# Performance work log

Measured on AMD Instinct MI355X. Metric: run time of the kernel, lower is better.

Reference implementation:

```python
import jax, jax.numpy as jnp
import numpy as np

N_HEADS = 16
EPSILON = 0.01
SCORE_SCALE = 1.0
C_CONST = 2.0 + EPSILON


def setup_inputs() -> dict:
    key = jax.random.key(0)
    k1, k2, k3 = jax.random.split(key, 3)
    B, T, D = 2, 2048, 1024
    x = jax.random.normal(k1, (B, T, D), dtype=jnp.float32)
    # torch nn.Linear convention: weight [out_features, in_features], y = x @ W.T
    Wqkv = jax.random.normal(k2, (3 * D, D), dtype=jnp.float32) * (1.0 / np.sqrt(D))
    Wout = jax.random.normal(k3, (D, D), dtype=jnp.float32) * (1.0 / np.sqrt(D))
    return {"x": x, "Wqkv": Wqkv, "Wout": Wout}


def reference(x, Wqkv, Wout):
    B, T, D = x.shape
    H = N_HEADS
    hd = D // H
    qkv = x @ Wqkv.T  # [B, T, 3D]
    q, k, v = jnp.split(qkv, 3, axis=-1)
    # [B, H, T, hd]
    q = q.reshape(B, T, H, hd).transpose(0, 2, 1, 3).astype(jnp.float32)
    k = k.reshape(B, T, H, hd).transpose(0, 2, 1, 3).astype(jnp.float32)
    v = v.reshape(B, T, H, hd).transpose(0, 2, 1, 3).astype(jnp.float32)
    # L2 normalize along head dim (F.normalize uses eps=1e-12 via clamp of norm)
    qn = q / jnp.maximum(jnp.linalg.norm(q, axis=-1, keepdims=True), 1e-12)
    kn = k / jnp.maximum(jnp.linalg.norm(k, axis=-1, keepdims=True), 1e-12)
    # full T x T kernel matrix per (batch, head)
    x_dot = jnp.einsum("bhtd,bhsd->bhts", qn, kn)
    denom = jnp.maximum(C_CONST - 2.0 * x_dot, 1e-6)
    K = (x_dot * x_dot) / denom * SCORE_SCALE
    causal = jnp.tril(jnp.ones((T, T), dtype=bool))  # keep lower triangle incl. diag
    K = jnp.where(causal[None, None, :, :], K, 0.0)
    numerator = jnp.einsum("bhts,bhsd->bhtd", K, v)
    denominator = jnp.sum(K, axis=-1, keepdims=True)
    out = numerator / (denominator + 1e-6)
    out = out.transpose(0, 2, 1, 3).reshape(B, T, D)
    return out @ Wout.T
```

## Files before the change

### kernel.cpp

```cpp
#include <hip/hip_runtime.h>
#include <hip/hip_bf16.h>

#define T_SEQ 2048
#define D_MODEL 1024
#define BT 4096
#define QKV_N 3072

typedef __attribute__((ext_vector_type(8))) short bf16x8;
typedef __attribute__((ext_vector_type(4))) short bf16x4;
typedef __attribute__((ext_vector_type(4))) float f32x4;

typedef unsigned int __attribute__((address_space(1))) as1_uint;
typedef unsigned int __attribute__((address_space(3))) as3_uint;

__device__ __forceinline__ unsigned short f2bf(float f) {
    unsigned u = __builtin_bit_cast(unsigned, f);
    u += 0x7fffu + ((u >> 16) & 1u);
    return (unsigned short)(u >> 16);
}
__device__ __forceinline__ float bf2f(unsigned short h) {
    unsigned u = ((unsigned)h) << 16;
    return __builtin_bit_cast(float, u);
}
__device__ __forceinline__ void gload_lds16(const void* g, void* l) {
    __builtin_amdgcn_global_load_lds((const as1_uint*)g, (as3_uint*)l, 16, 0, 0);
}
__device__ __forceinline__ unsigned cvtpk_bf16(float lo, float hi) {
    unsigned r;
    asm("v_cvt_pk_bf16_f32 %0, %1, %2" : "=v"(r) : "v"(lo), "v"(hi));
    return r;
}

__global__ __launch_bounds__(256) void cvt_bf16_3(const float* __restrict__ s0, unsigned short* __restrict__ d0, int n0,
                                                  const float* __restrict__ s1, unsigned short* __restrict__ d1, int n1,
                                                  const float* __restrict__ s2, unsigned short* __restrict__ d2, int n2) {
    int i = blockIdx.x * 256 + threadIdx.x;
    const float* s; unsigned short* d;
    if (i < n0) { s = s0; d = d0; }
    else if (i < n0 + n1) { i -= n0; s = s1; d = d1; }
    else if (i < n0 + n1 + n2) { i -= n0 + n1; s = s2; d = d2; }
    else return;
    const float4* sp = (const float4*)s + (size_t)i * 2;
    const float4 a = sp[0], b = sp[1];
    uint4 o;
    o.x = (unsigned)f2bf(a.x) | ((unsigned)f2bf(a.y) << 16);
    o.y = (unsigned)f2bf(a.z) | ((unsigned)f2bf(a.w) << 16);
    o.z = (unsigned)f2bf(b.x) | ((unsigned)f2bf(b.y) << 16);
    o.w = (unsigned)f2bf(b.z) | ((unsigned)f2bf(b.w) << 16);
    ((uint4*)d)[i] = o;
}

template<int MODE>
__global__ __launch_bounds__(256) void gemm_bt_mfma(const unsigned short* __restrict__ A,
                                                    const unsigned short* __restrict__ B,
                                                    void* __restrict__ Cout,
                                                    unsigned short* __restrict__ qbp,
                                                    unsigned short* __restrict__ kbp,
                                                    int M, int N, int K) {
    __shared__ unsigned short As[128 * 64];
    __shared__ unsigned short Bs[128 * 64];
    const int tid = threadIdx.x;
    const int w = tid >> 6;
    const int l = tid & 63;
    const int l15 = l & 15, l4 = l >> 4;

    const int nblocks = (M / 128) * (N / 128);
    const int cpx = nblocks >> 3;
    const int id2 = (blockIdx.x & 7) * cpx + (blockIdx.x >> 3);
    const int bm = (id2 & 31) * 128;
    const int bn = (id2 >> 5) * 128;

    const int wm = (w >> 1) * 64, wn = (w & 1) * 64;

    const f32x4 z = {0.f, 0.f, 0.f, 0.f};
    f32x4 acc[4][4];
#pragma unroll
    for (int m = 0; m < 4; ++m)
#pragma unroll
        for (int n = 0; n < 4; ++n) acc[m][n] = z;

    const int lrow = l >> 3;
    const int lslot = (l & 7) ^ (lrow & 7);

    for (int k0 = 0; k0 < K; k0 += 64) {
#pragma unroll
        for (int i = 0; i < 4; ++i) {
            const int row = w * 32 + i * 8 + lrow;
            gload_lds16(A + (size_t)(bm + row) * K + k0 + lslot * 8, As + (w * 4 + i) * 512);
            gload_lds16(B + (size_t)(bn + row) * K + k0 + lslot * 8, Bs + (w * 4 + i) * 512);
        }
        __syncthreads();
        bf16x8 af[4][2], bfr[4][2];
#pragma unroll
        for (int m = 0; m < 4; ++m) {
            const int row = wm + m * 16 + l15;
            af[m][0] = *(const bf16x8*)(As + row * 64 + ((l4 ^ (row & 7)) * 8));
            af[m][1] = *(const bf16x8*)(As + row * 64 + (((4 + l4) ^ (row & 7)) * 8));
        }
#pragma unroll
        for (int n = 0; n < 4; ++n) {
            const int row = wn + n * 16 + l15;
            bfr[n][0] = *(const bf16x8*)(Bs + row * 64 + ((l4 ^ (row & 7)) * 8));
            bfr[n][1] = *(const bf16x8*)(Bs + row * 64 + (((4 + l4) ^ (row & 7)) * 8));
        }
#pragma unroll
        for (int m = 0; m < 4; ++m)
#pragma unroll
            for (int n = 0; n < 4; ++n) {
                acc[m][n] = __builtin_amdgcn_mfma_f32_16x16x32_bf16(af[m][0], bfr[n][0], acc[m][n], 0, 0, 0);
                acc[m][n] = __builtin_amdgcn_mfma_f32_16x16x32_bf16(af[m][1], bfr[n][1], acc[m][n], 0, 0, 0);
            }
        __syncthreads();
    }

    if (MODE == 0) {
#pragma unroll
        for (int m = 0; m < 4; ++m)
#pragma unroll
            for (int n = 0; n < 4; ++n)
#pragma unroll
                for (int r = 0; r < 4; ++r) {
                    const int row = bm + wm + m * 16 + l4 * 4 + r;
                    const int col = bn + wn + n * 16 + l15;
                    ((float*)Cout)[(size_t)row * N + col] = acc[m][n][r];
                }
    } else {
        const int gcol0 = bn + wn;
        const int part = gcol0 >> 10;
        const int h = (gcol0 >> 6) & 15;
        if (part < 2) {
            unsigned short* dst = part ? kbp : qbp;
#pragma unroll
            for (int m = 0; m < 4; ++m)
#pragma unroll
                for (int r = 0; r < 4; ++r) {
                    float ss = 0.f;
#pragma unroll
                    for (int n = 0; n < 4; ++n) ss = fmaf(acc[m][n][r], acc[m][n][r], ss);
                    ss += __shfl_xor(ss, 1);
                    ss += __shfl_xor(ss, 2);
                    ss += __shfl_xor(ss, 4);
                    ss += __shfl_xor(ss, 8);
                    const float sc = 1.0f / fmaxf(sqrtf(ss), 1e-12f);
                    const int row = bm + wm + m * 16 + l4 * 4 + r;
                    const int bh2 = (row >> 11) * 16 + h;
                    unsigned short* pdst = dst + ((size_t)bh2 * T_SEQ + (row & 2047)) * 64 + l15;
#pragma unroll
                    for (int n = 0; n < 4; ++n) pdst[n * 16] = f2bf(acc[m][n][r] * sc);
                }
        } else {
            unsigned short* vrow = (unsigned short*)Cout;
            const int vcol0 = gcol0 - 2048;
#pragma unroll
            for (int m = 0; m < 4; ++m)
#pragma unroll
                for (int n = 0; n < 4; ++n)
#pragma unroll
                    for (int r = 0; r < 4; ++r) {
                        const int row = bm + wm + m * 16 + l4 * 4 + r;
                        vrow[(size_t)row * D_MODEL + vcol0 + n * 16 + l15] = f2bf(acc[m][n][r]);
                    }
        }
    }
}

__global__ __launch_bounds__(256) void v_cvt_T(const unsigned short* __restrict__ vrow,
                                               unsigned short* __restrict__ vbT) {
    __shared__ unsigned short tile[64][72];
    const int bh = blockIdx.y;
    const int b = bh >> 4, h = bh & 15;
    const int t0 = blockIdx.x * 64;
    const int r = threadIdx.x >> 2;
    const int c = (threadIdx.x & 3) * 16;
    const unsigned short* src = vrow + (size_t)(b * T_SEQ + t0 + r) * D_MODEL + h * 64 + c;
    uint4 v0 = *(const uint4*)(src);
    uint4 v1 = *(const uint4*)(src + 8);
    unsigned short tmp[16];
    *(uint4*)tmp = v0;
    *(uint4*)(tmp + 8) = v1;
#pragma unroll
    for (int j = 0; j < 16; ++j) tile[c + j][r] = tmp[j];
    __syncthreads();
    const int d = threadIdx.x >> 2;
    const int tc = (threadIdx.x & 3) * 16;
    const int t5 = tc >> 5, t4 = (tc >> 4) & 1;
    unsigned short* dstrow = vbT + ((size_t)bh * 64 + d) * T_SEQ + t0;
    const int dp = d & 7;
#pragma unroll
    for (int q = 0; q < 4; ++q) {
        unsigned short tmp2[4];
#pragma unroll
        for (int i = 0; i < 4; ++i) tmp2[i] = tile[d][tc + q * 4 + i];
        const int slot = (t5 * 4 + q) ^ dp;
        *(uint2*)(dstrow + slot * 8 + t4 * 4) = *(uint2*)tmp2;
    }
}

#define AT_TS 64

__global__ __launch_bounds__(256, 4) void attn_mfma(const unsigned short* __restrict__ qb,
                                                    const unsigned short* __restrict__ kb,
                                                    const unsigned short* __restrict__ vbT,
                                                    unsigned short* __restrict__ attnb) {
    __shared__ unsigned short Ks[2][64 * 64];
    __shared__ unsigned short Vs[2][64 * 64];

    const int tid = threadIdx.x;
    const int w = tid >> 6;
    const int l = tid & 63;
    const int l15 = l & 15, l4 = l >> 4;

    const int id = blockIdx.x;
    const int xcd = id & 7;
    const int within = id >> 3;
    const int hl = (((within >> 5) & 1) << 1) | (within & 1);
    const int vv = (((within >> 6) & 1) << 4) | (((within >> 4) & 1) << 3) |
                   (((within >> 3) & 1) << 2) | (((within >> 2) & 1) << 1) |
                   ((within >> 1) & 1);
    const int pfl = ((within >> 5) & 1) ^ (within & 1);
    const int bh = xcd * 4 + hl;
    const int t0i = pfl ? 31 - vv : vv;
    const int t0 = t0i * 64;

    const size_t hb = (size_t)bh * T_SEQ * 64;

    const int lrow = l >> 3;
    const int lslot = (l & 7) ^ (lrow & 7);
    const unsigned short* kgp[2];
    const unsigned short* vgp[2];
    unsigned short* kdst[2];
    unsigned short* vdst[2];
#pragma unroll
    for (int c = 0; c < 2; ++c) {
        const int row = w * 16 + c * 8 + lrow;
        kgp[c] = kb + hb + (size_t)row * 64 + lslot * 8;
        vgp[c] = vbT + hb + (size_t)row * T_SEQ + (l & 7) * 8;
        kdst[c] = &Ks[0][(w * 2 + c) * 512];
        vdst[c] = &Vs[0][(w * 2 + c) * 512];
    }

    const int p = l15 & 7;
    const unsigned short* kfp0 = &Ks[0][0] + l15 * 64 + ((l4 ^ p) * 8);
    const unsigned short* kfp1 = &Ks[0][0] + l15 * 64 + (((4 + l4) ^ p) * 8);
    const unsigned short* vfp0 = &Vs[0][0] + l15 * 64 + ((l4 ^ p) * 8);
    const unsigned short* vfp1 = &Vs[0][0] + l15 * 64 + (((4 + l4) ^ p) * 8);

    bf16x8 qf0, qf1;
    {
        const unsigned short* qp = qb + hb + (size_t)(t0 + w * 16 + l15) * 64 + l4 * 8;
        qf0 = *(const bf16x8*)(qp);
        qf1 = *(const bf16x8*)(qp + 32);
    }

    const f32x4 z = {0.f, 0.f, 0.f, 0.f};
    f32x4 acc[4];
#pragma unroll
    for (int i = 0; i < 4; ++i) acc[i] = z;
    float accd = 0.f;

    const int wrow0 = t0 + w * 16;
    const int tq = wrow0 + l15;

#pragma unroll
    for (int c = 0; c < 2; ++c) {
        gload_lds16(kgp[c], kdst[c]);
        gload_lds16(vgp[c], vdst[c]);
    }

    auto compute_tile = [&](int roff, int s0, bool mask) {
        const unsigned short* kc0 = kfp0 + roff;
        const unsigned short* kc1 = kfp1 + roff;
        f32x4 sC[4];
        __builtin_amdgcn_s_setprio(1);
#pragma unroll
        for (int sf = 0; sf < 4; ++sf) {
            bf16x8 kf0 = *(const bf16x8*)(kc0 + sf * 1024);
            bf16x8 kf1 = *(const bf16x8*)(kc1 + sf * 1024);
            f32x4 c = z;
            c = __builtin_amdgcn_mfma_f32_16x16x32_bf16(kf0, qf0, c, 0, 0, 0);
            c = __builtin_amdgcn_mfma_f32_16x16x32_bf16(kf1, qf1, c, 0, 0, 0);
            sC[sf] = c;
        }
        __builtin_amdgcn_s_setprio(0);
        float part_ = 0.f;
#pragma unroll
        for (int sf = 0; sf < 4; ++sf)
#pragma unroll
            for (int r = 0; r < 4; ++r) {
                const float xd = sC[sf][r];
                const float den = __builtin_fmaf(-2.0f, xd, 2.01f);
                float Kv = xd * xd * __builtin_amdgcn_rcpf(den);
                if (mask) {
                    const int s = s0 + sf * 16 + l4 * 4 + r;
                    if (s > tq) Kv = 0.f;
                }
                part_ += Kv;
                sC[sf][r] = Kv;
            }
        accd += part_;
        uint4 p0, p1;
        p0.x = cvtpk_bf16(sC[0][0], sC[0][1]);
        p0.y = cvtpk_bf16(sC[0][2], sC[0][3]);
        p0.z = cvtpk_bf16(sC[1][0], sC[1][1]);
        p0.w = cvtpk_bf16(sC[1][2], sC[1][3]);
        p1.x = cvtpk_bf16(sC[2][0], sC[2][1]);
        p1.y = cvtpk_bf16(sC[2][2], sC[2][3]);
        p1.z = cvtpk_bf16(sC[3][0], sC[3][1]);
        p1.w = cvtpk_bf16(sC[3][2], sC[3][3]);
        const bf16x8 a0 = __builtin_bit_cast(bf16x8, p0);
        const bf16x8 a1 = __builtin_bit_cast(bf16x8, p1);
        const unsigned short* vc0 = vfp0 + roff;
        const unsigned short* vc1 = vfp1 + roff;
        __builtin_amdgcn_s_setprio(1);
#pragma unroll
        for (int df = 0; df < 4; ++df) {
            const bf16x8 B0 = *(const bf16x8*)(vc0 + df * 1024);
            const bf16x8 B1 = *(const bf16x8*)(vc1 + df * 1024);
            acc[df] = __builtin_amdgcn_mfma_f32_16x16x32_bf16(a0, B0, acc[df], 0, 0, 0);
            acc[df] = __builtin_amdgcn_mfma_f32_16x16x32_bf16(a1, B1, acc[df], 0, 0, 0);
        }
        __builtin_amdgcn_s_setprio(0);
    };

    for (int st = 0; st < t0i; ++st) {
        const int dsto = ((st & 1) ^ 1) * 4096;
#pragma unroll
        for (int c = 0; c < 2; ++c) {
            kgp[c] += 4096;
            vgp[c] += 64;
            gload_lds16(kgp[c], kdst[c] + dsto);
            gload_lds16(vgp[c], vdst[c] + dsto);
        }
        asm volatile("s_waitcnt vmcnt(4)" ::: "memory");
        __builtin_amdgcn_sched_barrier(0);
        __builtin_amdgcn_s_barrier();
        compute_tile((st & 1) * 4096, st * AT_TS, false);
        __builtin_amdgcn_sched_barrier(0);
        __builtin_amdgcn_s_barrier();
    }
    {
        asm volatile("s_waitcnt vmcnt(0)" ::: "memory");
        __builtin_amdgcn_sched_barrier(0);
        __builtin_amdgcn_s_barrier();
        compute_tile((t0i & 1) * 4096, t0i * AT_TS, true);
    }

    accd += __shfl_xor(accd, 16);
    accd += __shfl_xor(accd, 32);

    const int b = bh >> 4, h = bh & 15;
#pragma unroll
    for (int r = 0; r < 4; ++r) {
        const float den = __shfl(accd, l4 * 4 + r) + 1e-6f;
#pragma unroll
        for (int df = 0; df < 4; ++df) {
            const int t = wrow0 + l4 * 4 + r;
            const float o = acc[df][r] / den;
            attnb[((size_t)b * T_SEQ + t) * D_MODEL + h * 64 + df * 16 + l15] = f2bf(o);
        }
    }
}

extern "C" void kernel_launch(void* const* d_in, const int* in_sizes, int n_in,
                              void* d_out, int out_size, void* d_ws, size_t ws_size,
                              hipStream_t stream) {
    const float* x    = (const float*)d_in[0];
    const float* Wqkv = (const float*)d_in[1];
    const float* Wout = (const float*)d_in[2];
    float* out = (float*)d_out;

    char* ws = (char*)d_ws;
    unsigned short* xb    = (unsigned short*)(ws);
    unsigned short* wqkvb = (unsigned short*)(ws + (size_t)8 * 1024 * 1024);
    unsigned short* vrow  = (unsigned short*)(ws + (size_t)16 * 1024 * 1024);
    unsigned short* vbT   = (unsigned short*)(ws + (size_t)24 * 1024 * 1024);
    unsigned short* woutb = (unsigned short*)(ws + (size_t)32 * 1024 * 1024);
    unsigned short* qbp   = (unsigned short*)(ws + (size_t)34 * 1024 * 1024);
    unsigned short* kbp   = (unsigned short*)(ws + (size_t)42 * 1024 * 1024);
    unsigned short* attnb = (unsigned short*)(ws + (size_t)50 * 1024 * 1024);

    cvt_bf16_3<<<4096, 256, 0, stream>>>(x, xb, BT * D_MODEL / 8,
                                         Wqkv, wqkvb, QKV_N * D_MODEL / 8,
                                         Wout, woutb, D_MODEL * D_MODEL / 8);

    gemm_bt_mfma<2><<<(QKV_N / 128) * (BT / 128), 256, 0, stream>>>(
        xb, wqkvb, vrow, qbp, kbp, BT, QKV_N, D_MODEL);

    v_cvt_T<<<dim3(T_SEQ / 64, 32), 256, 0, stream>>>(vrow, vbT);

    attn_mfma<<<1024, 256, 0, stream>>>(qbp, kbp, vbT, attnb);

    gemm_bt_mfma<0><<<(D_MODEL / 128) * (BT / 128), 256, 0, stream>>>(
        attnb, woutb, out, nullptr, nullptr, BT, D_MODEL, D_MODEL);
}
```

Measured before the change: 179.3 us.

## Split long causal attention rows into two KV chunks with a reduction kernel

The causal attention kernel now splits each query tile at positions 16 and above into two key/value chunks (split-K), so no block processes more than 16 KV tiles. A static task table orders the work longest-first to balance load across the 1536 blocks. The partial numerators (bf16) and denominators go to reused workspace buffers, and a new attn_reduce kernel combines and normalizes them. This adds an extra launch, extra memory traffic and bf16 rounding of the partial numerators.

```diff
diff --git a/kernel.cpp b/kernel.cpp
--- a/kernel.cpp
+++ b/kernel.cpp
@@ -198,10 +198,22 @@
 
 #define AT_TS 64
 
+static __device__ const unsigned char task_tab[48] = {
+    (15<<1)|0,(16<<1)|0,(17<<1)|0,(18<<1)|0,(19<<1)|0,(20<<1)|0,(21<<1)|0,(22<<1)|0,
+    (23<<1)|0,(24<<1)|0,(25<<1)|0,(26<<1)|0,(27<<1)|0,(28<<1)|0,(29<<1)|0,(30<<1)|0,
+    (31<<1)|0,(31<<1)|1,
+    (14<<1)|0,(30<<1)|1,(13<<1)|0,(29<<1)|1,(12<<1)|0,(28<<1)|1,(11<<1)|0,(27<<1)|1,
+    (10<<1)|0,(26<<1)|1,(9<<1)|0,(25<<1)|1,(8<<1)|0,(24<<1)|1,(7<<1)|0,(23<<1)|1,
+    (6<<1)|0,(22<<1)|1,(5<<1)|0,(21<<1)|1,(4<<1)|0,(20<<1)|1,(3<<1)|0,(19<<1)|1,
+    (2<<1)|0,(18<<1)|1,(1<<1)|0,(17<<1)|1,(0<<1)|0,(16<<1)|1,
+};
+
 __global__ __launch_bounds__(256, 4) void attn_mfma(const unsigned short* __restrict__ qb,
                                                     const unsigned short* __restrict__ kb,
                                                     const unsigned short* __restrict__ vbT,
-                                                    unsigned short* __restrict__ attnb) {
+                                                    unsigned short* __restrict__ attnb,
+                                                    unsigned short* __restrict__ pnum,
+                                                    float* __restrict__ pden) {
     __shared__ unsigned short Ks[2][64 * 64];
     __shared__ unsigned short Vs[2][64 * 64];
 
@@ -212,15 +224,17 @@
 
     const int id = blockIdx.x;
     const int xcd = id & 7;
-    const int within = id >> 3;
-    const int hl = (((within >> 5) & 1) << 1) | (within & 1);
-    const int vv = (((within >> 6) & 1) << 4) | (((within >> 4) & 1) << 3) |
-                   (((within >> 3) & 1) << 2) | (((within >> 2) & 1) << 1) |
-                   ((within >> 1) & 1);
-    const int pfl = ((within >> 5) & 1) ^ (within & 1);
+    const int wq = id >> 3;
+    const int hl = wq & 3;
+    const int task = wq >> 2;
     const int bh = xcd * 4 + hl;
-    const int t0i = pfl ? 31 - vv : vv;
-    const int t0 = t0i * 64;
+    const int tv = task_tab[task];
+    const int j = tv >> 1;
+    const int chunk = tv & 1;
+    const int nst = chunk ? (j - 15) : (j < 16 ? j + 1 : 16);
+    const bool mfin = chunk ? true : (j < 16);
+    const int s_base = chunk * 16;
+    const int t0 = j * 64;
 
     const size_t hb = (size_t)bh * T_SEQ * 64;
 
@@ -233,8 +247,8 @@
 #pragma unroll
     for (int c = 0; c < 2; ++c) {
         const int row = w * 16 + c * 8 + lrow;
-        kgp[c] = kb + hb + (size_t)row * 64 + lslot * 8;
-        vgp[c] = vbT + hb + (size_t)row * T_SEQ + (l & 7) * 8;
+        kgp[c] = kb + hb + (size_t)(s_base * 64 + row) * 64 + lslot * 8;
+        vgp[c] = vbT + hb + (size_t)row * T_SEQ + s_base * 64 + (l & 7) * 8;
         kdst[c] = &Ks[0][(w * 2 + c) * 512];
         vdst[c] = &Vs[0][(w * 2 + c) * 512];
     }
@@ -322,7 +336,7 @@
         __builtin_amdgcn_s_setprio(0);
     };
 
-    for (int st = 0; st < t0i; ++st) {
+    for (int st = 0; st < nst - 1; ++st) {
         const int dsto = ((st & 1) ^ 1) * 4096;
 #pragma unroll
         for (int c = 0; c < 2; ++c) {
@@ -334,7 +348,7 @@
         asm volatile("s_waitcnt vmcnt(4)" ::: "memory");
         __builtin_amdgcn_sched_barrier(0);
         __builtin_amdgcn_s_barrier();
-        compute_tile((st & 1) * 4096, st * AT_TS, false);
+        compute_tile((st & 1) * 4096, (s_base + st) * AT_TS, false);
         __builtin_amdgcn_sched_barrier(0);
         __builtin_amdgcn_s_barrier();
     }
@@ -342,23 +356,62 @@
         asm volatile("s_waitcnt vmcnt(0)" ::: "memory");
         __builtin_amdgcn_sched_barrier(0);
         __builtin_amdgcn_s_barrier();
-        compute_tile((t0i & 1) * 4096, t0i * AT_TS, true);
+        compute_tile(((nst - 1) & 1) * 4096, (s_base + nst - 1) * AT_TS, mfin);
     }
 
     accd += __shfl_xor(accd, 16);
     accd += __shfl_xor(accd, 32);
 
+    if (!chunk && j < 16) {
+        const int b = bh >> 4, h = bh & 15;
+#pragma unroll
+        for (int r = 0; r < 4; ++r) {
+            const float den = __shfl(accd, l4 * 4 + r) + 1e-6f;
+#pragma unroll
+            for (int df = 0; df < 4; ++df) {
+                const int t = wrow0 + l4 * 4 + r;
+                const float o = acc[df][r] / den;
+                attnb[((size_t)b * T_SEQ + t) * D_MODEL + h * 64 + df * 16 + l15] = f2bf(o);
+            }
+        }
+    } else {
+        const int pj = j - 16;
+        const int pidx = (bh * 16 + pj) * 2 + chunk;
+        unsigned short* np = pnum + (size_t)pidx * 4096;
+#pragma unroll
+        for (int r = 0; r < 4; ++r)
+#pragma unroll
+            for (int df = 0; df < 4; ++df)
+                np[(w * 16 + l4 * 4 + r) * 64 + df * 16 + l15] = f2bf(acc[df][r]);
+        if (l4 == 0) pden[pidx * 64 + w * 16 + l15] = accd;
+    }
+}
+
+__global__ __launch_bounds__(256) void attn_reduce(const unsigned short* __restrict__ pnum,
+                                                   const float* __restrict__ pden,
+                                                   unsigned short* __restrict__ attnb) {
+    const int bh = blockIdx.y;
+    const int jj = blockIdx.x;
+    const int row = threadIdx.x >> 2;
+    const int d0 = (threadIdx.x & 3) * 16;
+    const int pi = (bh * 16 + jj) * 2;
+    const float den = pden[pi * 64 + row] + pden[(pi + 1) * 64 + row] + 1e-6f;
+    const float inv = 1.0f / den;
+    const unsigned short* n0 = pnum + (size_t)pi * 4096 + row * 64 + d0;
+    const unsigned short* n1 = n0 + 4096;
     const int b = bh >> 4, h = bh & 15;
-#pragma unroll
-    for (int r = 0; r < 4; ++r) {
-        const float den = __shfl(accd, l4 * 4 + r) + 1e-6f;
-#pragma unroll
-        for (int df = 0; df < 4; ++df) {
-            const int t = wrow0 + l4 * 4 + r;
-            const float o = acc[df][r] / den;
-            attnb[((size_t)b * T_SEQ + t) * D_MODEL + h * 64 + df * 16 + l15] = f2bf(o);
-        }
-    }
+    unsigned short* dst = attnb + ((size_t)b * T_SEQ + (16 + jj) * 64 + row) * D_MODEL + h * 64 + d0;
+    uint4 a0 = *(const uint4*)n0, a1 = *(const uint4*)(n0 + 8);
+    uint4 c0 = *(const uint4*)n1, c1 = *(const uint4*)(n1 + 8);
+    unsigned short sa[8], sb[8], o[16];
+    *(uint4*)sa = a0; *(uint4*)sb = c0;
+#pragma unroll
+    for (int i = 0; i < 8; ++i) o[i] = f2bf((bf2f(sa[i]) + bf2f(sb[i])) * inv);
+    *(uint4*)sa = a1; *(uint4*)sb = c1;
+#pragma unroll
+    for (int i = 0; i < 8; ++i) o[8 + i] = f2bf((bf2f(sa[i]) + bf2f(sb[i])) * inv);
+    *(uint4*)dst = *(uint4*)o;
+    *(uint4*)(dst + 8) = *(uint4*)(o + 8);
 }
 
 extern "C" void kernel_launch(void* const* d_in, const int* in_sizes, int n_in,
@@ -378,6 +431,8 @@
     unsigned short* qbp   = (unsigned short*)(ws + (size_t)34 * 1024 * 1024);
     unsigned short* kbp   = (unsigned short*)(ws + (size_t)42 * 1024 * 1024);
     unsigned short* attnb = (unsigned short*)(ws + (size_t)50 * 1024 * 1024);
+    unsigned short* pnum  = xb;
+    float*          pden  = (float*)vrow;
 
     cvt_bf16_3<<<4096, 256, 0, stream>>>(x, xb, BT * D_MODEL / 8,
                                          Wqkv, wqkvb, QKV_N * D_MODEL / 8,
@@ -388,7 +443,9 @@
 
     v_cvt_T<<<dim3(T_SEQ / 64, 32), 256, 0, stream>>>(vrow, vbT);
 
-    attn_mfma<<<1024, 256, 0, stream>>>(qbp, kbp, vbT, attnb);
+    attn_mfma<<<1536, 256, 0, stream>>>(qbp, kbp, vbT, attnb, pnum, pden);
+
+    attn_reduce<<<dim3(16, 32), 256, 0, stream>>>(pnum, pden, attnb);
 
     gemm_bt_mfma<0><<<(D_MODEL / 128) * (BT / 128), 256, 0, stream>>>(
         attnb, woutb, out, nullptr, nullptr, BT, D_MODEL, D_MODEL);
```

Result: faster. 175.6 us (-2.0%).
